# Kernel tuning notes

Measured on AMD Instinct MI355X. Metric: run time of the kernel, lower is better.

Reference implementation:

```python
import jax, jax.numpy as jnp
import numpy as np

B, C, N = 8, 64, 8192
H, D = 4, 64  # num_heads, dim per head


def setup_inputs() -> dict:
    key = jax.random.key(0)
    ks = jax.random.split(key, 6)
    feat = jax.random.normal(ks[0], (B, C, N, 3), dtype=jnp.float32)
    xyz = jax.random.normal(ks[1], (B, N, 3), dtype=jnp.float32)
    # VNLinear weights: (out_channels, in_channels), xavier-uniform-ish scale
    def xavier(k, o, i):
        lim = (6.0 / (o + i)) ** 0.5
        return jax.random.uniform(k, (o, i), dtype=jnp.float32, minval=-lim, maxval=lim)
    Wq = xavier(ks[2], H * D, C)
    Wk = xavier(ks[3], H * D, C)
    Wv = xavier(ks[4], H * D, C)
    Wout = xavier(ks[5], C, H * D)
    return {"feat": feat, "xyz": xyz, "Wq": Wq, "Wk": Wk, "Wv": Wv, "Wout": Wout}


def reference(feat, xyz, Wq, Wk, Wv, Wout):
    b, c, n, _ = feat.shape
    # VNLinear: einsum('bind,oi->bond')
    q = jnp.einsum('bind,oi->bond', feat, Wq).reshape(b, H, D, n, 3)
    k = jnp.einsum('bind,oi->bond', feat, Wk).reshape(b, H, D, n, 3)
    v = jnp.einsum('bind,oi->bond', feat, Wv).reshape(b, H, D, n, 3)
    # NOTE: contracts over d and f(=N); attn is [B,H,3,3] (attention over xyz axes)
    attn = jnp.einsum('bhdfn,bhdfm->bhnm', q, k)
    attn = jax.nn.softmax(attn / (D * 3.0) ** 0.5, axis=-1)
    out = jnp.einsum('bhnm,bhdfm->bhdfn', attn, v).reshape(b, H * D, n, 3)
    return jnp.einsum('bind,oi->bond', out, Wout) + feat
```

## Files before the change

### kernel.cpp

```cpp
#include <hip/hip_runtime.h>
#include <math.h>

typedef _Float16 f16;
typedef _Float16 f16x8 __attribute__((ext_vector_type(8)));
typedef _Float16 f16x4 __attribute__((ext_vector_type(4)));
typedef float f32x4 __attribute__((ext_vector_type(4)));

#define BATCH 8
#define CHN   64
#define NPTS  8192
#define P2    192
#define GG    (P2 * P2)
#define NCHG  32

__global__ __launch_bounds__(256) void k_w(const float* __restrict__ Wq,
                                           const float* __restrict__ Wk,
                                           const float* __restrict__ Wv,
                                           const float* __restrict__ Wout,
                                           float* __restrict__ P,
                                           float* __restrict__ MX) {
    __shared__ float WL[16384 + 256];
    const int blk = blockIdx.x;
    const int tid = threadIdx.x;

    if (blk < 4) {
        const int h = blk;
        float* WoutL = WL;
        float* WvL   = WL + 4096;
        for (int i = tid; i < 4096; i += 256) {
            int r = i >> 6, cd = i & 63;
            WoutL[i] = Wout[r * 256 + h * 64 + cd];
            WvL[i]   = Wv[(h * 64 + r) * 64 + cd];
        }
        __syncthreads();
        for (int e = 0; e < 16; e++) {
            int id = e * 256 + tid;
            int r = id >> 6, c2 = id & 63;
            float s = 0.0f;
#pragma unroll 8
            for (int d = 0; d < 64; d++)
                s += WoutL[r * 64 + d] * WvL[d * 64 + c2];
            P[h * 4096 + id] = s;
        }
    } else {
        const int p = blk - 4;
        const int c = p / 3;
        float* WkL   = WL;
        float* WqCol = WL + 16384;
        for (int i = tid; i < 16384; i += 256)
            WkL[i] = Wk[i];
        if (tid < 256)
            WqCol[tid] = Wq[tid * 64 + c];
        __syncthreads();
        if (tid < P2) {
            const int q2 = tid, c2 = q2 / 3;
            f32x4 v;
#pragma unroll
            for (int h = 0; h < 4; h++) {
                float s = 0.0f;
#pragma unroll 8
                for (int d = 0; d < 64; d++)
                    s += WqCol[h * 64 + d] * WkL[(h * 64 + d) * 64 + c2];
                v[h] = s;
            }
            *(f32x4*)(MX + ((size_t)p * P2 + q2) * 4) = v;
        }
    }
}

__global__ __launch_bounds__(512, 2) void k_gram(const float* __restrict__ feat,
                                                 const f32x4* __restrict__ MX,
                                                 float* __restrict__ pl) {
    const int kc  = blockIdx.x & (NCHG - 1);
    const int b   = blockIdx.x >> 5;
    const int n0  = kc * 256;
    const int tid = threadIdx.x;
    const int wid = tid >> 6, lane = tid & 63;
    const int l15 = lane & 15, l4 = lane >> 4;
    const int qd = wid & 3, strip = wid >> 2;
    const int qp = (qd >> 1) * 96 + strip * 48;
    const int qq = (qd & 1) * 96;

    __shared__ char smem[77184];
    __shared__ float fin[8][36];
    char* T0 = smem;
    char* T1 = smem + 24576;
    float (*SRED)[36][67] = (float (*)[36][67])smem;

    const float* fb = feat + (size_t)b * CHN * NPTS * 3;
    const int tc = tid >> 4;
    const int g4 = (tid & 15) * 4;
    const int g8 = (tid & 15) * 8;

    f32x4 acc[3][6];
#pragma unroll
    for (int i = 0; i < 3; i++)
#pragma unroll
        for (int j = 0; j < 6; j++) acc[i][j] = (f32x4){0.f, 0.f, 0.f, 0.f};

    float4 SA[2][3], SB[2][3];

#define G_LOADS(S, nbase)                                                      \
    {                                                                          \
        _Pragma("unroll")                                                      \
        for (int ti = 0; ti < 2; ti++) {                                       \
            int c = tc + ti * 32;                                              \
            const float* src = fb + ((size_t)c * NPTS + (nbase) + g4) * 3;     \
            S[ti][0] = *(const float4*)(src);                                  \
            S[ti][1] = *(const float4*)(src + 4);                              \
            S[ti][2] = *(const float4*)(src + 8);                              \
        }                                                                      \
    }
#define G_WRITES(S, Tb)                                                        \
    {                                                                          \
        _Pragma("unroll")                                                      \
        for (int ti = 0; ti < 2; ti++) {                                       \
            int c = tc + ti * 32;                                              \
            float v[12] = {S[ti][0].x, S[ti][0].y, S[ti][0].z, S[ti][0].w,     \
                           S[ti][1].x, S[ti][1].y, S[ti][1].z, S[ti][1].w,     \
                           S[ti][2].x, S[ti][2].y, S[ti][2].z, S[ti][2].w};    \
            _Pragma("unroll")                                                  \
            for (int t = 0; t < 3; t++) {                                      \
                int row = c * 3 + t;                                           \
                f16x4 pk = {(f16)v[t], (f16)v[3 + t], (f16)v[6 + t],           \
                            (f16)v[9 + t]};                                    \
                int bo = (row * 128 + g8) ^ ((row & 7) << 4);                  \
                *(f16x4*)((Tb) + bo) = pk;                                     \
            }                                                                  \
        }                                                                      \
    }
#define G_COMPUTE(Tb)                                                          \
    {                                                                          \
        _Pragma("unroll")                                                      \
        for (int ks = 0; ks < 2; ks++) {                                       \
            f16x8 af[3], bf[6];                                                \
            _Pragma("unroll")                                                  \
            for (int mt = 0; mt < 3; mt++) {                                   \
                int row = qp + mt * 16 + l15;                                  \
                af[mt] = *(const f16x8*)((Tb) +                                \
                    ((row * 128 + ks * 64 + l4 * 16) ^ ((row & 7) << 4)));     \
            }                                                                  \
            _Pragma("unroll")                                                  \
            for (int nt = 0; nt < 6; nt++) {                                   \
                int row = qq + nt * 16 + l15;                                  \
                bf[nt] = *(const f16x8*)((Tb) +                                \
                    ((row * 128 + ks * 64 + l4 * 16) ^ ((row & 7) << 4)));     \
            }                                                                  \
            _Pragma("unroll")                                                  \
            for (int mt = 0; mt < 3; mt++)                                     \
                _Pragma("unroll")                                              \
                for (int nt = 0; nt < 6; nt++)                                 \
                    acc[mt][nt] = __builtin_amdgcn_mfma_f32_16x16x32_f16(      \
                        af[mt], bf[nt], acc[mt][nt], 0, 0, 0);                 \
        }                                                                      \
    }

    G_LOADS(SA, n0);
    G_WRITES(SA, T0);
    G_LOADS(SB, n0 + 64);
    __syncthreads();
    G_COMPUTE(T0); G_WRITES(SB, T1); G_LOADS(SA, n0 + 128);
    __syncthreads();
    G_COMPUTE(T1); G_WRITES(SA, T0); G_LOADS(SB, n0 + 192);
    __syncthreads();
    G_COMPUTE(T0); G_WRITES(SB, T1);
    __syncthreads();
    G_COMPUTE(T1);
    __syncthreads();

    float l[36];
#pragma unroll
    for (int i = 0; i < 36; i++) l[i] = 0.0f;
#pragma unroll
    for (int mt = 0; mt < 3; mt++) {
#pragma unroll
        for (int r = 0; r < 4; r++) {
            int p = qp + mt * 16 + l4 * 4 + r;
            const f32x4* mxp = MX + (size_t)p * P2 + qq + l15;
#pragma unroll
            for (int nt = 0; nt < 6; nt++) {
                f32x4 ms = mxp[nt * 16];
                float g = acc[mt][nt][r];
                const int ts = ((mt + r) % 3) * 3 + (nt % 3);
                l[ts]      = fmaf(ms[0], g, l[ts]);
                l[9 + ts]  = fmaf(ms[1], g, l[9 + ts]);
                l[18 + ts] = fmaf(ms[2], g, l[18 + ts]);
                l[27 + ts] = fmaf(ms[3], g, l[27 + ts]);
            }
        }
    }
    const int pt = l4 % 3, ps = l15 % 3;
    int rowmap[9];
#pragma unroll
    for (int tt = 0; tt < 3; tt++)
#pragma unroll
        for (int ss = 0; ss < 3; ss++)
            rowmap[tt * 3 + ss] = ((tt + pt) % 3) * 3 + ((ss + ps) % 3);
#pragma unroll
    for (int h = 0; h < 4; h++)
#pragma unroll
        for (int i9 = 0; i9 < 9; i9++)
            SRED[wid][h * 9 + rowmap[i9]][lane] = l[h * 9 + i9];
    __syncthreads();
    if (tid < 288) {
        int w = tid / 36, row = tid - (tid / 36) * 36;
        float s = 0.0f;
#pragma unroll 8
        for (int col = 0; col < 64; col++) s += SRED[w][row][col];
        fin[w][row] = s;
    }
    __syncthreads();
    if (tid < 36) {
        float s = 0.0f;
#pragma unroll
        for (int w = 0; w < 8; w++) s += fin[w][tid];
        pl[(size_t)(b * NCHG + kc) * 36 + tid] = s;
    }
#undef G_LOADS
#undef G_WRITES
#undef G_COMPUTE
}

__global__ __launch_bounds__(256) void k_abig(const float* __restrict__ pl,
                                              const float* __restrict__ P,
                                              f16* __restrict__ Ab) {
    const int blk = blockIdx.x;
    const int b   = blk / 144;
    const int tid = threadIdx.x;
    __shared__ float ls[36], wsm[36];
    if (tid < 36) {
        float s = 0.0f;
        for (int k = 0; k < NCHG; k++)
            s += pl[(size_t)(b * NCHG + k) * 36 + tid];
        ls[tid] = s * 0.07216878364870322f;
    }
    __syncthreads();
    if (tid < 36) {
        int base = (tid / 3) * 3;
        float z0 = ls[base], z1 = ls[base + 1], z2 = ls[base + 2];
        float mx = fmaxf(z0, fmaxf(z1, z2));
        float e0 = expf(z0 - mx), e1 = expf(z1 - mx), e2 = expf(z2 - mx);
        wsm[tid] = expf(ls[tid] - mx) / (e0 + e1 + e2);
    }
    __syncthreads();

    int i  = blk * 256 + tid;
    int rr = i - b * GG;
    int p2 = rr / P2, q2 = rr - p2 * P2;
    int o = p2 / 3, t = p2 - 3 * (p2 / 3);
    int c = q2 / 3, s = q2 - 3 * (q2 / 3);
    float acc = (p2 == q2) ? 1.0f : 0.0f;
#pragma unroll
    for (int h = 0; h < 4; h++)
        acc = fmaf(wsm[h * 9 + t * 3 + s], P[h * 4096 + o * 64 + c], acc);
    Ab[i] = (f16)acc;
}

__global__ __launch_bounds__(256, 4) void k_apply(const float* __restrict__ feat,
                                                  const f16* __restrict__ Ab,
                                                  float* __restrict__ out) {
    const int nb  = blockIdx.x & 127;
    const int b   = blockIdx.x >> 7;
    const int n0  = nb * 64;
    const int tid = threadIdx.x;
    const int wid = tid >> 6, lane = tid & 63;
    const int l15 = lane & 15, l4 = lane >> 4;

    __shared__ char lds[25600];

    const float* fb = feat + (size_t)b * CHN * NPTS * 3;
    const f16*   A  = Ab + (size_t)b * GG;
    float*       ob = out + (size_t)b * CHN * NPTS * 3;

    {
        float4 S[12];
#pragma unroll
        for (int i = 0; i < 12; i++) {
            int idx = tid + i * 256;
            int c = idx / 48, j = idx - (idx / 48) * 48;
            S[i] = *(const float4*)(fb + ((size_t)c * NPTS + n0) * 3 + j * 4);
        }
#pragma unroll
        for (int i = 0; i < 12; i++) {
            int idx = tid + i * 256;
            int c = idx / 48, j = idx - (idx / 48) * 48;
            float vv[4] = {S[i].x, S[i].y, S[i].z, S[i].w};
#pragma unroll
            for (int u = 0; u < 4; u++) {
                int e = j * 4 + u, nn = e / 3, s = e - 3 * (e / 3);
                *(f16*)(lds + nn * 400 + (c * 3 + s) * 2) = (f16)vv[u];
            }
        }
    }
    __syncthreads();

    f32x4 acc[3][4];
#pragma unroll
    for (int i = 0; i < 3; i++)
#pragma unroll
        for (int j = 0; j < 4; j++) acc[i][j] = (f32x4){0.f, 0.f, 0.f, 0.f};

    f16x8 afA[3], afB[3];
    const int prow = wid * 48 + l15;

#define LOAD_AF(dst, ks)                                                       \
    {                                                                          \
        _Pragma("unroll")                                                      \
        for (int mt = 0; mt < 3; mt++)                                         \
            dst[mt] = *(const f16x8*)(A + (size_t)(prow + mt * 16) * P2        \
                                        + (ks) * 32 + l4 * 8);                 \
    }
#define DO_MFMA(src, ks)                                                       \
    {                                                                          \
        f16x8 bf[4];                                                           \
        _Pragma("unroll")                                                      \
        for (int nt = 0; nt < 4; nt++) {                                       \
            int nl = nt * 16 + l15;                                            \
            bf[nt] = *(const f16x8*)(lds + nl * 400 + (ks) * 64 + l4 * 16);    \
        }                                                                      \
        _Pragma("unroll")                                                      \
        for (int mt = 0; mt < 3; mt++)                                         \
            _Pragma("unroll")                                                  \
            for (int nt = 0; nt < 4; nt++)                                     \
                acc[mt][nt] = __builtin_amdgcn_mfma_f32_16x16x32_f16(          \
                    src[mt], bf[nt], acc[mt][nt], 0, 0, 0);                    \
    }

    LOAD_AF(afA, 0);
    LOAD_AF(afB, 1); DO_MFMA(afA, 0);
    LOAD_AF(afA, 2); DO_MFMA(afB, 1);
    LOAD_AF(afB, 3); DO_MFMA(afA, 2);
    LOAD_AF(afA, 4); DO_MFMA(afB, 3);
    LOAD_AF(afB, 5); DO_MFMA(afA, 4);
    DO_MFMA(afB, 5);
#undef LOAD_AF
#undef DO_MFMA

    __syncthreads();

#pragma unroll
    for (int rnd = 0; rnd < 2; rnd++) {
#pragma unroll
        for (int mt = 0; mt < 3; mt++) {
#pragma unroll
            for (int r = 0; r < 4; r++) {
                int p2 = wid * 48 + mt * 16 + l4 * 4 + r;
                int o = p2 / 3, t = p2 - 3 * (p2 / 3);
#pragma unroll
                for (int ntl = 0; ntl < 2; ntl++) {
                    int nnl = ntl * 16 + l15;
                    *(float*)(lds + o * 400 + (nnl * 3 + t) * 4)
                        = acc[mt][rnd * 2 + ntl][r];
                }
            }
        }
        __syncthreads();
#pragma unroll
        for (int k = 0; k < 6; k++) {
            int fid = k * 256 + tid;
            int o = fid / 24, w = fid - (fid / 24) * 24;
            float4 v = *(const float4*)(lds + o * 400 + w * 16);
            *(float4*)(ob + ((size_t)o * NPTS + n0 + rnd * 32) * 3 + w * 4) = v;
        }
        __syncthreads();
    }
}

extern "C" void kernel_launch(void* const* d_in, const int* in_sizes, int n_in,
                              void* d_out, int out_size, void* d_ws, size_t ws_size,
                              hipStream_t stream) {
    const float* feat = (const float*)d_in[0];
    const float* Wq   = (const float*)d_in[2];
    const float* Wk   = (const float*)d_in[3];
    const float* Wv   = (const float*)d_in[4];
    const float* Wout = (const float*)d_in[5];
    float* out = (float*)d_out;

    char* w8 = (char*)d_ws;
    f16*   Ab = (f16*)w8;
    float* P  = (float*)(w8 + 589824);
    float* MX = (float*)(w8 + 655360);
    float* pl = (float*)(w8 + 1245184);

    k_w    <<<196,          256, 0, stream>>>(Wq, Wk, Wv, Wout, P, MX);
    k_gram <<<BATCH * NCHG, 512, 0, stream>>>(feat, (const f32x4*)MX, pl);
    k_abig <<<1152,         256, 0, stream>>>(pl, P, Ab);
    k_apply<<<1024,         256, 0, stream>>>(feat, Ab, out);
}
```

Before: 62.23 us.

## Split gram kernel into more N-chunks and store MX projection in fp16

The Gram kernel now handles 128 points per block instead of 256, doubling the grid to 512 blocks so that, with two blocks allowed per CU, all CUs have work. Each block runs two pipelined stages instead of four. The MX mixing matrix is stored in fp16 to halve its footprint and the bandwidth of the per-block epilogue reads. The cost is twice as many partial results for the downstream reduction to sum, and reduced precision in the mixing coefficients.

```diff
diff --git a/kernel.cpp b/kernel.cpp
--- a/kernel.cpp
+++ b/kernel.cpp
@@ -11,14 +11,14 @@
 #define NPTS  8192
 #define P2    192
 #define GG    (P2 * P2)
-#define NCHG  32
+#define NCHG  64
 
 __global__ __launch_bounds__(256) void k_w(const float* __restrict__ Wq,
                                            const float* __restrict__ Wk,
                                            const float* __restrict__ Wv,
                                            const float* __restrict__ Wout,
                                            float* __restrict__ P,
-                                           float* __restrict__ MX) {
+                                           f16* __restrict__ MX) {
     __shared__ float WL[16384 + 256];
     const int blk = blockIdx.x;
     const int tid = threadIdx.x;
@@ -54,26 +54,26 @@
         __syncthreads();
         if (tid < P2) {
             const int q2 = tid, c2 = q2 / 3;
-            f32x4 v;
+            f16x4 v;
 #pragma unroll
             for (int h = 0; h < 4; h++) {
                 float s = 0.0f;
 #pragma unroll 8
                 for (int d = 0; d < 64; d++)
                     s += WqCol[h * 64 + d] * WkL[(h * 64 + d) * 64 + c2];
-                v[h] = s;
+                v[h] = (f16)s;
             }
-            *(f32x4*)(MX + ((size_t)p * P2 + q2) * 4) = v;
+            *(f16x4*)(MX + ((size_t)p * P2 + q2) * 4) = v;
         }
     }
 }
 
 __global__ __launch_bounds__(512, 2) void k_gram(const float* __restrict__ feat,
-                                                 const f32x4* __restrict__ MX,
+                                                 const f16x4* __restrict__ MX,
                                                  float* __restrict__ pl) {
     const int kc  = blockIdx.x & (NCHG - 1);
-    const int b   = blockIdx.x >> 5;
-    const int n0  = kc * 256;
+    const int b   = blockIdx.x >> 6;
+    const int n0  = kc * 128;
     const int tid = threadIdx.x;
     const int wid = tid >> 6, lane = tid & 63;
     const int l15 = lane & 15, l4 = lane >> 4;
@@ -159,10 +159,6 @@
     G_WRITES(SA, T0);
     G_LOADS(SB, n0 + 64);
     __syncthreads();
-    G_COMPUTE(T0); G_WRITES(SB, T1); G_LOADS(SA, n0 + 128);
-    __syncthreads();
-    G_COMPUTE(T1); G_WRITES(SA, T0); G_LOADS(SB, n0 + 192);
-    __syncthreads();
     G_COMPUTE(T0); G_WRITES(SB, T1);
     __syncthreads();
     G_COMPUTE(T1);
@@ -176,16 +172,16 @@
 #pragma unroll
         for (int r = 0; r < 4; r++) {
             int p = qp + mt * 16 + l4 * 4 + r;
-            const f32x4* mxp = MX + (size_t)p * P2 + qq + l15;
+            const f16x4* mxp = MX + (size_t)p * P2 + qq + l15;
 #pragma unroll
             for (int nt = 0; nt < 6; nt++) {
-                f32x4 ms = mxp[nt * 16];
+                f16x4 ms = mxp[nt * 16];
                 float g = acc[mt][nt][r];
                 const int ts = ((mt + r) % 3) * 3 + (nt % 3);
-                l[ts]      = fmaf(ms[0], g, l[ts]);
-                l[9 + ts]  = fmaf(ms[1], g, l[9 + ts]);
-                l[18 + ts] = fmaf(ms[2], g, l[18 + ts]);
-                l[27 + ts] = fmaf(ms[3], g, l[27 + ts]);
+                l[ts]      = fmaf((float)ms[0], g, l[ts]);
+                l[9 + ts]  = fmaf((float)ms[1], g, l[9 + ts]);
+                l[18 + ts] = fmaf((float)ms[2], g, l[18 + ts]);
+                l[27 + ts] = fmaf((float)ms[3], g, l[27 + ts]);
             }
         }
     }
@@ -379,11 +375,11 @@
     char* w8 = (char*)d_ws;
     f16*   Ab = (f16*)w8;
     float* P  = (float*)(w8 + 589824);
-    float* MX = (float*)(w8 + 655360);
-    float* pl = (float*)(w8 + 1245184);
+    f16*   MX = (f16*)(w8 + 655360);
+    float* pl = (float*)(w8 + 950272);
 
     k_w    <<<196,          256, 0, stream>>>(Wq, Wk, Wv, Wout, P, MX);
-    k_gram <<<BATCH * NCHG, 512, 0, stream>>>(feat, (const f32x4*)MX, pl);
+    k_gram <<<BATCH * NCHG, 512, 0, stream>>>(feat, (const f16x4*)MX, pl);
     k_abig <<<1152,         256, 0, stream>>>(pl, P, Ab);
     k_apply<<<1024,         256, 0, stream>>>(feat, Ab, out);
 }
```

Result: slower. 68.66 us (+10.3%).

## Compact Wq^T Wk mixing matrix to 64x64 fp16 and stage it in LDS

Applied to the files above, without the earlier changes.

The per-head Wq^T·Wk product is now computed once as a 64x64x4 matrix in k_w, using 4 blocks instead of 192, rather than expanded into a 192x192x4 fp32 table. k_gram loads this 32KB fp16 table into shared memory and indexes it by channel (p/3, q/3) during the epilogue, which removes large global reads per block. The cost is an extra 32KB of LDS per block, which may reduce occupancy at 2 blocks of 512 threads, plus fp16 rounding of the mixing coefficients and integer divides for the indexing.

```diff
diff --git a/kernel.cpp b/kernel.cpp
--- a/kernel.cpp
+++ b/kernel.cpp
@@ -18,8 +18,8 @@
                                            const float* __restrict__ Wv,
                                            const float* __restrict__ Wout,
                                            float* __restrict__ P,
-                                           float* __restrict__ MX) {
-    __shared__ float WL[16384 + 256];
+                                           f16* __restrict__ MS) {
+    __shared__ float WL[8192];
     const int blk = blockIdx.x;
     const int tid = threadIdx.x;
 
@@ -43,33 +43,29 @@
             P[h * 4096 + id] = s;
         }
     } else {
-        const int p = blk - 4;
-        const int c = p / 3;
-        float* WkL   = WL;
-        float* WqCol = WL + 16384;
-        for (int i = tid; i < 16384; i += 256)
-            WkL[i] = Wk[i];
-        if (tid < 256)
-            WqCol[tid] = Wq[tid * 64 + c];
+        const int h = blk - 4;
+        float* WqL = WL;
+        float* WkL = WL + 4096;
+        for (int i = tid; i < 4096; i += 256) {
+            int d = i >> 6, cc = i & 63;
+            WqL[i] = Wq[(h * 64 + d) * 64 + cc];
+            WkL[i] = Wk[(h * 64 + d) * 64 + cc];
+        }
         __syncthreads();
-        if (tid < P2) {
-            const int q2 = tid, c2 = q2 / 3;
-            f32x4 v;
-#pragma unroll
-            for (int h = 0; h < 4; h++) {
-                float s = 0.0f;
+        for (int e = 0; e < 16; e++) {
+            int id = e * 256 + tid;
+            int c = id >> 6, c2 = id & 63;
+            float s = 0.0f;
 #pragma unroll 8
-                for (int d = 0; d < 64; d++)
-                    s += WqCol[h * 64 + d] * WkL[(h * 64 + d) * 64 + c2];
-                v[h] = s;
-            }
-            *(f32x4*)(MX + ((size_t)p * P2 + q2) * 4) = v;
+            for (int d = 0; d < 64; d++)
+                s += WqL[d * 64 + c] * WkL[d * 64 + c2];
+            MS[(size_t)id * 4 + h] = (f16)s;
         }
     }
 }
 
 __global__ __launch_bounds__(512, 2) void k_gram(const float* __restrict__ feat,
-                                                 const f32x4* __restrict__ MX,
+                                                 const f16x4* __restrict__ MS,
                                                  float* __restrict__ pl) {
     const int kc  = blockIdx.x & (NCHG - 1);
     const int b   = blockIdx.x >> 5;
@@ -83,6 +79,7 @@
 
     __shared__ char smem[77184];
     __shared__ float fin[8][36];
+    __shared__ f16x4 MSL[4096];
     char* T0 = smem;
     char* T1 = smem + 24576;
     float (*SRED)[36][67] = (float (*)[36][67])smem;
@@ -91,6 +88,9 @@
     const int tc = tid >> 4;
     const int g4 = (tid & 15) * 4;
     const int g8 = (tid & 15) * 8;
+
+    for (int i = tid; i < 4096; i += 512)
+        MSL[i] = MS[i];
 
     f32x4 acc[3][6];
 #pragma unroll
@@ -168,6 +168,11 @@
     G_COMPUTE(T1);
     __syncthreads();
 
+    int c2v[6];
+#pragma unroll
+    for (int nt = 0; nt < 6; nt++)
+        c2v[nt] = (qq + l15 + nt * 16) / 3;
+
     float l[36];
 #pragma unroll
     for (int i = 0; i < 36; i++) l[i] = 0.0f;
@@ -176,16 +181,17 @@
 #pragma unroll
         for (int r = 0; r < 4; r++) {
             int p = qp + mt * 16 + l4 * 4 + r;
-            const f32x4* mxp = MX + (size_t)p * P2 + qq + l15;
+            int c = p / 3;
+            const f16x4* mrow = &MSL[c * 64];
 #pragma unroll
             for (int nt = 0; nt < 6; nt++) {
-                f32x4 ms = mxp[nt * 16];
+                f16x4 ms = mrow[c2v[nt]];
                 float g = acc[mt][nt][r];
                 const int ts = ((mt + r) % 3) * 3 + (nt % 3);
-                l[ts]      = fmaf(ms[0], g, l[ts]);
-                l[9 + ts]  = fmaf(ms[1], g, l[9 + ts]);
-                l[18 + ts] = fmaf(ms[2], g, l[18 + ts]);
-                l[27 + ts] = fmaf(ms[3], g, l[27 + ts]);
+                l[ts]      = fmaf((float)ms[0], g, l[ts]);
+                l[9 + ts]  = fmaf((float)ms[1], g, l[9 + ts]);
+                l[18 + ts] = fmaf((float)ms[2], g, l[18 + ts]);
+                l[27 + ts] = fmaf((float)ms[3], g, l[27 + ts]);
             }
         }
     }
@@ -379,11 +385,11 @@
     char* w8 = (char*)d_ws;
     f16*   Ab = (f16*)w8;
     float* P  = (float*)(w8 + 589824);
-    float* MX = (float*)(w8 + 655360);
-    float* pl = (float*)(w8 + 1245184);
-
-    k_w    <<<196,          256, 0, stream>>>(Wq, Wk, Wv, Wout, P, MX);
-    k_gram <<<BATCH * NCHG, 512, 0, stream>>>(feat, (const f32x4*)MX, pl);
+    f16*   MS = (f16*)(w8 + 655360);
+    float* pl = (float*)(w8 + 688128);
+
+    k_w    <<<8,            256, 0, stream>>>(Wq, Wk, Wv, Wout, P, MS);
+    k_gram <<<BATCH * NCHG, 512, 0, stream>>>(feat, (const f16x4*)MS, pl);
     k_abig <<<1152,         256, 0, stream>>>(pl, P, Ab);
     k_apply<<<1024,         256, 0, stream>>>(feat, Ab, out);
 }
```

After: 58.95 us. 1.06x faster.
